# Kernel tuning notes

Hardware: AMD Instinct MI355X
Metric: run time of the kernel (lower is better)

The kernel has to match this reference:

```python
import jax, jax.numpy as jnp
import numpy as np

B, N_O, N_Q = 2, 512, 512
POS_DIM, LATENT, HEADS, HEAD_DIM, OUT_DIM = 3, 256, 8, 32, 128
HD = HEADS * HEAD_DIM  # == LATENT here


def _lin(key, fan_in, fan_out):
    return jax.random.normal(key, (fan_in, fan_out), jnp.float32) / np.sqrt(fan_in)


def setup_inputs() -> dict:
    key = jax.random.key(0)
    ks = jax.random.split(key, 12)
    return {
        'h_obs': jax.random.normal(ks[0], (B, N_O, LATENT), jnp.float32),
        'pos_obs': jax.random.uniform(ks[1], (B, N_O, POS_DIM), jnp.float32),
        'pos_query': jax.random.uniform(ks[2], (B, N_Q, POS_DIM), jnp.float32),
        'fw1': _lin(ks[3], LATENT, LATENT), 'fb1': jnp.zeros((LATENT,), jnp.float32),
        'fw2': _lin(ks[4], LATENT, HD), 'fb2': jnp.zeros((HD,), jnp.float32),
        'log_sigma': jnp.zeros((HEADS,), jnp.float32),
        'kw1': _lin(ks[5], POS_DIM * 3, LATENT), 'kb1': jnp.zeros((LATENT,), jnp.float32),
        'kw2': _lin(ks[6], LATENT, HEADS), 'kb2': jnp.zeros((HEADS,), jnp.float32),
        'ow': _lin(ks[7], HD, OUT_DIM), 'ob': jnp.zeros((OUT_DIM,), jnp.float32),
        'vw': _lin(ks[8], HD, OUT_DIM), 'vb': jnp.zeros((OUT_DIM,), jnp.float32),
    }


def reference(h_obs, pos_obs, pos_query, fw1, fb1, fw2, fb2, log_sigma,
              kw1, kb1, kw2, kb2, ow, ob, vw, vb):
    Bv, No, _ = h_obs.shape
    Nq = pos_query.shape[1]
    # feature net -> values [B, H, N_o, D]
    v = jax.nn.relu(h_obs @ fw1 + fb1) @ fw2 + fb2
    v = v.reshape(Bv, No, HEADS, HEAD_DIM).transpose(0, 2, 1, 3)
    # pairwise relative positions [B, Nq, No, P]
    pos_q = pos_query[:, :, None, :]
    pos_o = pos_obs[:, None, :, :]
    rel = pos_q - pos_o
    dist2 = jnp.sum(rel ** 2, axis=-1)  # [B, Nq, No]
    sigma = jnp.exp(log_sigma)[None, :, None, None]
    rbf = jnp.exp(-dist2[:, None] / (sigma ** 2 + 1e-6))  # [B, H, Nq, No]
    # kernel MLP on concatenated pairwise positions [B, Nq, No, 3P] -> [B, H, Nq, No]
    ki = jnp.concatenate([
        jnp.broadcast_to(pos_q, (Bv, Nq, No, POS_DIM)),
        jnp.broadcast_to(pos_o, (Bv, Nq, No, POS_DIM)),
        rel], axis=-1)
    delta = (jax.nn.relu(ki @ kw1 + kb1) @ kw2 + kb2).transpose(0, 3, 1, 2)
    logits = jnp.log(rbf + 1e-8) + delta
    weights = jax.nn.softmax(logits, axis=-1)  # [B, H, Nq, No]
    # weighted mean over observations
    v_mean = jnp.einsum('bhqo,bhod->bhqd', weights, v)  # [B, H, Nq, D]
    h_query = v_mean.transpose(0, 2, 1, 3).reshape(Bv, Nq, HD)
    # weighted variance: sum_o w * (v_o - v_mean)^2
    residual = v[:, :, None, :, :] - v_mean[:, :, :, None, :]  # [B, H, Nq, No, D]
    var = jnp.sum(weights[..., None] * residual ** 2, axis=3)  # [B, H, Nq, D]
    var = var.transpose(0, 2, 1, 3).reshape(Bv, Nq, HD)
    mean = h_query @ ow + ob
    var_out = jax.nn.softplus(var @ vw + vb)
    return (mean, var_out)
```

## Files before the change

kernel.cpp:

```cpp
#include <hip/hip_runtime.h>
#include <math.h>

#define NB 2
#define NO 512
#define NQ 512
#define OUT_DIM 128
#define LPAD 520

typedef __attribute__((ext_vector_type(8))) short short8;
typedef __attribute__((ext_vector_type(4))) float f32x4;
typedef float v2f __attribute__((ext_vector_type(2)));

__device__ __forceinline__ float softplus_f(float x) {
  return x > 0.0f ? x + log1pf(expf(-x)) : log1pf(expf(x));
}
__device__ __forceinline__ unsigned short bf16_rne(float f) {
  unsigned u = __float_as_uint(f);
  unsigned r = u + 0x7FFFu + ((u >> 16) & 1u);
  return (unsigned short)(r >> 16);
}
__device__ __forceinline__ float bf16_to_f32(unsigned short h) {
  return __uint_as_float(((unsigned)h) << 16);
}
__device__ __forceinline__ unsigned pack_bf2(float x, float y) {
  unsigned ux = __float_as_uint(x);
  unsigned uy = __float_as_uint(y);
  ux = ux + 0x7FFFu + ((ux >> 16) & 1u);
  uy = uy + 0x7FFFu + ((uy >> 16) & 1u);
  return (ux >> 16) | (uy & 0xFFFF0000u);
}
__device__ __forceinline__ v2f unpk_bf2(unsigned u) {
  v2f r; r.x = __uint_as_float(u << 16); r.y = __uint_as_float(u & 0xFFFF0000u);
  return r;
}
__device__ __forceinline__ v2f splat2(float x) { v2f r; r.x = x; r.y = x; return r; }
__device__ __forceinline__ v2f fma2(v2f a, v2f b, v2f c) { return __builtin_elementwise_fma(a, b, c); }
__device__ __forceinline__ v2f max2(v2f a, v2f b) { return __builtin_elementwise_max(a, b); }

__global__ __launch_bounds__(1024) void prep_kernel(
    const float* __restrict__ h_obs, const float* __restrict__ fw1,
    const float* __restrict__ fb1, const float* __restrict__ fw2,
    const float* __restrict__ fb2, const float* __restrict__ pos_obs,
    const float* __restrict__ kw1, unsigned short* __restrict__ V_bf,
    unsigned short* __restrict__ AO_bf)
{
  if (blockIdx.x < 256) {
    __shared__ float s_red[4][4][256];
    __shared__ float s_hid[4][256];
    const int n  = threadIdx.x & 255;
    const int ks = threadIdx.x >> 8;
    const int r0 = blockIdx.x * 4;
    const int k0 = ks * 64;
    float a0 = 0.f, a1 = 0.f, a2 = 0.f, a3 = 0.f;
    #pragma unroll 8
    for (int kk = 0; kk < 64; ++kk) {
      int k = k0 + kk;
      float w = fw1[k * 256 + n];
      a0 = fmaf(h_obs[(r0 + 0) * 256 + k], w, a0);
      a1 = fmaf(h_obs[(r0 + 1) * 256 + k], w, a1);
      a2 = fmaf(h_obs[(r0 + 2) * 256 + k], w, a2);
      a3 = fmaf(h_obs[(r0 + 3) * 256 + k], w, a3);
    }
    s_red[ks][0][n] = a0; s_red[ks][1][n] = a1;
    s_red[ks][2][n] = a2; s_red[ks][3][n] = a3;
    __syncthreads();
    if (ks == 0) {
      float bb = fb1[n];
      #pragma unroll
      for (int r = 0; r < 4; ++r) {
        float v = s_red[0][r][n] + s_red[1][r][n] + s_red[2][r][n] + s_red[3][r][n] + bb;
        s_hid[r][n] = fmaxf(v, 0.f);
      }
    }
    __syncthreads();
    float c0 = 0.f, c1 = 0.f, c2 = 0.f, c3 = 0.f;
    #pragma unroll 8
    for (int kk = 0; kk < 64; ++kk) {
      int k = k0 + kk;
      float w = fw2[k * 256 + n];
      c0 = fmaf(s_hid[0][k], w, c0);
      c1 = fmaf(s_hid[1][k], w, c1);
      c2 = fmaf(s_hid[2][k], w, c2);
      c3 = fmaf(s_hid[3][k], w, c3);
    }
    __syncthreads();
    s_red[ks][0][n] = c0; s_red[ks][1][n] = c1;
    s_red[ks][2][n] = c2; s_red[ks][3][n] = c3;
    __syncthreads();
    if (ks == 0) {
      float bb = fb2[n];
      #pragma unroll
      for (int r = 0; r < 4; ++r) {
        float v = s_red[0][r][n] + s_red[1][r][n] + s_red[2][r][n] + s_red[3][r][n] + bb;
        V_bf[(size_t)(r0 + r) * 256 + n] = bf16_rne(v);
      }
    }
  } else {
    const int i  = blockIdx.x - 256;
    const int b  = i >> 7;
    const int og = i & 127;
    const int ol = threadIdx.x >> 8;
    const int j  = threadIdx.x & 255;
    const int o  = og * 4 + ol;
    float c0 = kw1[3 * 256 + j] - kw1[6 * 256 + j];
    float c1 = kw1[4 * 256 + j] - kw1[7 * 256 + j];
    float c2 = kw1[5 * 256 + j] - kw1[8 * 256 + j];
    const float* p = pos_obs + ((size_t)(b * NO + o)) * 3;
    AO_bf[(size_t)(b * NO + o) * 256 + j] =
        bf16_rne(fmaf(p[0], c0, fmaf(p[1], c1, p[2] * c2)));
  }
}

__global__ __launch_bounds__(512, 4) void attn_fused(
    const unsigned short* __restrict__ V_bf,
    const unsigned short* __restrict__ AO_bf,
    const float* __restrict__ kw1,
    const float* __restrict__ kb1,
    const float* __restrict__ kw2,
    const float* __restrict__ kb2,
    const float* __restrict__ log_sigma,
    const float* __restrict__ pos_obs,
    const float* __restrict__ pos_query,
    const float* __restrict__ ow, const float* __restrict__ obias,
    const float* __restrict__ vw, const float* __restrict__ vbias,
    float* __restrict__ out)
{
  __shared__ float s_logits[2][8 * LPAD];
  __shared__ __align__(16) char poolA[18432];
  __shared__ __align__(16) char poolB[4096];
  __shared__ float s_sum[2][8];

  short8* Bhi    = (short8*)poolA;
  short8* Blo    = (short8*)(poolA + 8192);
  float*  s_redA = (float*)poolA;
  float*  s_pred = (float*)poolA;
  float*  s_aq   = (float*)poolB;
  float*  s_hv   = (float*)poolB;

  const int t   = threadIdx.x;
  const int bq0 = blockIdx.x * 2;
  const int b   = bq0 >> 9;

  float pqx[2], pqy[2], pqz[2];
  #pragma unroll
  for (int q = 0; q < 2; ++q) {
    pqx[q] = pos_query[(bq0 + q) * 3 + 0];
    pqy[q] = pos_query[(bq0 + q) * 3 + 1];
    pqz[q] = pos_query[(bq0 + q) * 3 + 2];
  }
  {
    const int q = t >> 8, j = t & 255;
    float c0 = kw1[0 * 256 + j] + kw1[6 * 256 + j];
    float c1 = kw1[1 * 256 + j] + kw1[7 * 256 + j];
    float c2 = kw1[2 * 256 + j] + kw1[8 * 256 + j];
    s_aq[q * 256 + j] =
        fmaf(pqx[q], c0, fmaf(pqy[q], c1, fmaf(pqz[q], c2, kb1[j])));
  }
  {
    const int o = t;
    const float* p = pos_obs + (size_t)(b * NO + o) * 3;
    float px = p[0], py = p[1], pz = p[2];
    float d2q[2];
    #pragma unroll
    for (int q = 0; q < 2; ++q) {
      float r0 = pqx[q] - px, r1 = pqy[q] - py, r2 = pqz[q] - pz;
      d2q[q] = r0 * r0 + r1 * r1 + r2 * r2;
    }
    #pragma unroll
    for (int h = 0; h < 8; ++h) {
      float sg  = expf(log_sigma[h]);
      float inv = 1.0f / (sg * sg + 1e-6f);
      float kbv = kb2[h];
      s_logits[0][h * LPAD + o] = logf(expf(-d2q[0] * inv) + 1e-8f) + kbv;
      s_logits[1][h * LPAD + o] = logf(expf(-d2q[1] * inv) + 1e-8f) + kbv;
    }
  }
  {
    const int kstep = t >> 6, lane = t & 63;
    const int nh = lane & 15;
    const int kb_ = kstep * 32 + ((lane >> 4) & 3) * 8;
    short8 hi8, lo8;
    #pragma unroll
    for (int i = 0; i < 8; ++i) {
      float v = (nh < 8) ? kw2[(kb_ + i) * 8 + nh] : 0.f;
      unsigned short h = bf16_rne(v);
      hi8[i] = (short)h;
      lo8[i] = (short)bf16_rne(v - bf16_to_f32(h));
    }
    Bhi[kstep * 64 + lane] = hi8;
    Blo[kstep * 64 + lane] = lo8;
  }
  __syncthreads();

  {
    const int wave = t >> 6, lane = t & 63;
    const int quad = lane >> 4, mrow = lane & 15;
    const int tb   = wave * 4;
    f32x4 C[2][4];
    #pragma unroll
    for (int q = 0; q < 2; ++q)
      #pragma unroll
      for (int jt = 0; jt < 4; ++jt) C[q][jt] = (f32x4){0.f, 0.f, 0.f, 0.f};

    for (int kstep = 0; kstep < 8; ++kstep) {
      const int koff = kstep * 32 + quad * 8;
      const v2f* aqp0 = (const v2f*)(s_aq + koff);
      const v2f* aqp1 = (const v2f*)(s_aq + 256 + koff);
      v2f aq0[4], aq1[4];
      #pragma unroll
      for (int i = 0; i < 4; ++i) { aq0[i] = aqp0[i]; aq1[i] = aqp1[i]; }
      short8 bhi = Bhi[kstep * 64 + lane];
      short8 blo = Blo[kstep * 64 + lane];
      #pragma unroll
      for (int jt = 0; jt < 4; ++jt) {
        const int o = (tb + jt) * 16 + mrow;
        int4 u = *(const int4*)(AO_bf + ((size_t)(b * NO + o) << 8) + koff);
        v2f ao[4];
        ao[0] = unpk_bf2((unsigned)u.x); ao[1] = unpk_bf2((unsigned)u.y);
        ao[2] = unpk_bf2((unsigned)u.z); ao[3] = unpk_bf2((unsigned)u.w);
        v2f z = splat2(0.f);
        int4 af0, af1;
        {
          v2f h0 = max2(aq0[0] + ao[0], z), h1 = max2(aq0[1] + ao[1], z);
          v2f h2 = max2(aq0[2] + ao[2], z), h3 = max2(aq0[3] + ao[3], z);
          af0.x = (int)pack_bf2(h0.x, h0.y); af0.y = (int)pack_bf2(h1.x, h1.y);
          af0.z = (int)pack_bf2(h2.x, h2.y); af0.w = (int)pack_bf2(h3.x, h3.y);
        }
        {
          v2f h0 = max2(aq1[0] + ao[0], z), h1 = max2(aq1[1] + ao[1], z);
          v2f h2 = max2(aq1[2] + ao[2], z), h3 = max2(aq1[3] + ao[3], z);
          af1.x = (int)pack_bf2(h0.x, h0.y); af1.y = (int)pack_bf2(h1.x, h1.y);
          af1.z = (int)pack_bf2(h2.x, h2.y); af1.w = (int)pack_bf2(h3.x, h3.y);
        }
        short8 a0 = __builtin_bit_cast(short8, af0);
        short8 a1 = __builtin_bit_cast(short8, af1);
        C[0][jt] = __builtin_amdgcn_mfma_f32_16x16x32_bf16(a0, bhi, C[0][jt], 0, 0, 0);
        C[0][jt] = __builtin_amdgcn_mfma_f32_16x16x32_bf16(a0, blo, C[0][jt], 0, 0, 0);
        C[1][jt] = __builtin_amdgcn_mfma_f32_16x16x32_bf16(a1, bhi, C[1][jt], 0, 0, 0);
        C[1][jt] = __builtin_amdgcn_mfma_f32_16x16x32_bf16(a1, blo, C[1][jt], 0, 0, 0);
      }
    }
    const int h = lane & 15;
    if (h < 8) {
      #pragma unroll
      for (int q = 0; q < 2; ++q)
        #pragma unroll
        for (int jt = 0; jt < 4; ++jt) {
          const int ob = (tb + jt) * 16 + quad * 4;
          #pragma unroll
          for (int r = 0; r < 4; ++r)
            s_logits[q][h * LPAD + ob + r] += C[q][jt][r];
        }
    }
  }
  __syncthreads();

  {
    const int wave = t >> 6, lane = t & 63;
    #pragma unroll
    for (int cc = 0; cc < 2; ++cc) {
      const int c = wave * 2 + cc;
      const int q = c >> 3, h = c & 7;
      float* pl = &s_logits[q][h * LPAD];
      float l[8];
      float m = -1e30f;
      #pragma unroll
      for (int k = 0; k < 8; ++k) {
        l[k] = pl[k * 64 + lane];
        m = fmaxf(m, l[k]);
      }
      #pragma unroll
      for (int off = 32; off >= 1; off >>= 1) m = fmaxf(m, __shfl_xor(m, off, 64));
      float s = 0.f;
      #pragma unroll
      for (int k = 0; k < 8; ++k) {
        float p = expf(l[k] - m);
        pl[k * 64 + lane] = p;
        s += p;
      }
      #pragma unroll
      for (int off = 32; off >= 1; off >>= 1) s += __shfl_xor(s, off, 64);
      if (lane == 0) s_sum[q][h] = s;
    }
  }
  __syncthreads();

  float q1p[8];
  {
    const int s  = t >> 6;
    const int r  = t & 63;
    const int h  = r >> 3, dg = r & 7;
    const unsigned short* vb_ = V_bf + ((size_t)(b * NO) << 8) + h * 32 + dg * 4;
    const float* P0 = &s_logits[0][h * LPAD];
    const float* P1 = &s_logits[1][h * LPAD];
    v2f s1a0 = splat2(0.f), s1b0 = splat2(0.f), s2a0 = splat2(0.f), s2b0 = splat2(0.f);
    v2f s1a1 = splat2(0.f), s1b1 = splat2(0.f), s2a1 = splat2(0.f), s2b1 = splat2(0.f);
    const int o0 = s * 64;
    #pragma unroll 4
    for (int oi = 0; oi < 64; ++oi) {
      const int o = o0 + oi;
      uint2 vv = *(const uint2*)(vb_ + ((size_t)o << 8));
      v2f va  = unpk_bf2(vv.x);
      v2f vb2 = unpk_bf2(vv.y);
      v2f p0 = splat2(P0[o]), p1 = splat2(P1[o]);
      s1a0 = fma2(p0, va, s1a0);  s1b0 = fma2(p0, vb2, s1b0);
      v2f t0a = p0 * va, t0b = p0 * vb2;
      s2a0 = fma2(t0a, va, s2a0); s2b0 = fma2(t0b, vb2, s2b0);
      s1a1 = fma2(p1, va, s1a1);  s1b1 = fma2(p1, vb2, s1b1);
      v2f t1a = p1 * va, t1b = p1 * vb2;
      s2a1 = fma2(t1a, va, s2a1); s2b1 = fma2(t1b, vb2, s2b1);
    }
    float* row = s_redA + t * 9;
    row[0] = s1a0.x; row[1] = s1a0.y; row[2] = s1b0.x; row[3] = s1b0.y;
    row[4] = s2a0.x; row[5] = s2a0.y; row[6] = s2b0.x; row[7] = s2b0.y;
    q1p[0] = s1a1.x; q1p[1] = s1a1.y; q1p[2] = s1b1.x; q1p[3] = s1b1.y;
    q1p[4] = s2a1.x; q1p[5] = s2a1.y; q1p[6] = s2b1.x; q1p[7] = s2b1.y;
  }
  __syncthreads();
  if (t < 256) {
    const int hd = t, h = hd >> 5, d = hd & 31, dg = d >> 2, c = d & 3;
    float S1 = 0.f, S2 = 0.f;
    #pragma unroll
    for (int s = 0; s < 8; ++s) {
      const float* row = s_redA + (size_t)(s * 64 + h * 8 + dg) * 9;
      S1 += row[c]; S2 += row[4 + c];
    }
    float inv = 1.0f / s_sum[0][h];
    float m1 = S1 * inv;
    float va = fmaxf(S2 * inv - m1 * m1, 0.f);
    s_hv[0 * 256 + hd] = m1;
    s_hv[1 * 256 + hd] = va;
  }
  __syncthreads();
  {
    float* row = s_redA + t * 9;
    #pragma unroll
    for (int i = 0; i < 8; ++i) row[i] = q1p[i];
  }
  __syncthreads();
  if (t < 256) {
    const int hd = t, h = hd >> 5, d = hd & 31, dg = d >> 2, c = d & 3;
    float S1 = 0.f, S2 = 0.f;
    #pragma unroll
    for (int s = 0; s < 8; ++s) {
      const float* row = s_redA + (size_t)(s * 64 + h * 8 + dg) * 9;
      S1 += row[c]; S2 += row[4 + c];
    }
    float inv = 1.0f / s_sum[1][h];
    float m1 = S1 * inv;
    float va = fmaxf(S2 * inv - m1 * m1, 0.f);
    s_hv[2 * 256 + hd] = m1;
    s_hv[3 * 256 + hd] = va;
  }
  __syncthreads();

  {
    const int ks = t >> 8, mode = (t >> 7) & 1, n = t & 127;
    const float* W  = mode ? vw : ow;
    const float* X0 = s_hv + mode * 256;
    const float* X1 = s_hv + (2 + mode) * 256;
    float a0 = 0.f, a1 = 0.f;
    const int k0 = ks * 128;
    #pragma unroll 4
    for (int k = k0; k < k0 + 128; k += 4) {
      float4 x0 = *(const float4*)&X0[k];
      float4 x1 = *(const float4*)&X1[k];
      float w0 = W[(k + 0) * 128 + n];
      float w1 = W[(k + 1) * 128 + n];
      float w2 = W[(k + 2) * 128 + n];
      float w3 = W[(k + 3) * 128 + n];
      a0 = fmaf(x0.x, w0, a0); a1 = fmaf(x1.x, w0, a1);
      a0 = fmaf(x0.y, w1, a0); a1 = fmaf(x1.y, w1, a1);
      a0 = fmaf(x0.z, w2, a0); a1 = fmaf(x1.z, w2, a1);
      a0 = fmaf(x0.w, w3, a0); a1 = fmaf(x1.w, w3, a1);
    }
    __syncthreads();
    s_pred[((ks * 2 + mode) * 2 + 0) * 128 + n] = a0;
    s_pred[((ks * 2 + mode) * 2 + 1) * 128 + n] = a1;
  }
  __syncthreads();
  {
    const int q = t >> 8, mode = (t >> 7) & 1, n = t & 127;
    float v = s_pred[((0 * 2 + mode) * 2 + q) * 128 + n]
            + s_pred[((1 * 2 + mode) * 2 + q) * 128 + n]
            + (mode ? vbias[n] : obias[n]);
    if (mode) v = softplus_f(v);
    out[(size_t)mode * (NB * NQ * OUT_DIM) + (size_t)(bq0 + q) * OUT_DIM + n] = v;
  }
}

extern "C" void kernel_launch(void* const* d_in, const int* in_sizes, int n_in,
                              void* d_out, int out_size, void* d_ws, size_t ws_size,
                              hipStream_t stream)
{
  const float* h_obs     = (const float*)d_in[0];
  const float* pos_obs   = (const float*)d_in[1];
  const float* pos_query = (const float*)d_in[2];
  const float* fw1       = (const float*)d_in[3];
  const float* fb1       = (const float*)d_in[4];
  const float* fw2       = (const float*)d_in[5];
  const float* fb2       = (const float*)d_in[6];
  const float* log_sigma = (const float*)d_in[7];
  const float* kw1       = (const float*)d_in[8];
  const float* kb1       = (const float*)d_in[9];
  const float* kw2       = (const float*)d_in[10];
  const float* kb2       = (const float*)d_in[11];
  const float* ow        = (const float*)d_in[12];
  const float* ob        = (const float*)d_in[13];
  const float* vw        = (const float*)d_in[14];
  const float* vb        = (const float*)d_in[15];

  float* out = (float*)d_out;
  unsigned short* ws = (unsigned short*)d_ws;

  unsigned short* V_bf  = ws;
  unsigned short* AO_bf = ws + 262144;

  prep_kernel<<<512, 1024, 0, stream>>>(h_obs, fw1, fb1, fw2, fb2,
                                        pos_obs, kw1, V_bf, AO_bf);
  attn_fused<<<NB * NQ / 2, 512, 0, stream>>>(V_bf, AO_bf, kw1, kb1, kw2, kb2,
                                              log_sigma, pos_obs, pos_query,
                                              ow, ob, vw, vb, out);
}
```

Measured before the change: 148.6 us.

## Shrink shared memory and retune prep and attention kernels for occupancy

The prep kernel is reorganized into 1024 blocks of 512 threads, each handling two rows instead of four. The attention kernel raises its launch-bounds occupancy hint to 6 and trims shared memory by changing LPAD and poolA size. It also caches the per-head sigma and bias terms in shared memory, vectorizes the probability loads as float4, and switches the partial-sum reduction to a column-major layout. Other changes include a hardware packed-bf16 conversion builtin and moving one barrier. These target occupancy and LDS bank conflicts, but the occupancy hint risks register spills.

```diff
diff --git a/kernel.cpp b/kernel.cpp
--- a/kernel.cpp
+++ b/kernel.cpp
@@ -5,7 +5,7 @@
 #define NO 512
 #define NQ 512
 #define OUT_DIM 128
-#define LPAD 520
+#define LPAD 516
 
 typedef __attribute__((ext_vector_type(8))) short short8;
 typedef __attribute__((ext_vector_type(4))) float f32x4;
@@ -22,12 +22,25 @@
 __device__ __forceinline__ float bf16_to_f32(unsigned short h) {
   return __uint_as_float(((unsigned)h) << 16);
 }
+
+#if defined(__has_builtin)
+#if __has_builtin(__builtin_amdgcn_cvt_pk_bf16_f32)
+#define HAS_CVT_PK_BF16 1
+#endif
+#endif
+
 __device__ __forceinline__ unsigned pack_bf2(float x, float y) {
+#ifdef HAS_CVT_PK_BF16
+  auto r = __builtin_amdgcn_cvt_pk_bf16_f32(x, y);
+  unsigned u; __builtin_memcpy(&u, &r, 4);
+  return u;
+#else
   unsigned ux = __float_as_uint(x);
   unsigned uy = __float_as_uint(y);
   ux = ux + 0x7FFFu + ((ux >> 16) & 1u);
   uy = uy + 0x7FFFu + ((uy >> 16) & 1u);
   return (ux >> 16) | (uy & 0xFFFF0000u);
+#endif
 }
 __device__ __forceinline__ v2f unpk_bf2(unsigned u) {
   v2f r; r.x = __uint_as_float(u << 16); r.y = __uint_as_float(u & 0xFFFF0000u);
@@ -37,71 +50,59 @@
 __device__ __forceinline__ v2f fma2(v2f a, v2f b, v2f c) { return __builtin_elementwise_fma(a, b, c); }
 __device__ __forceinline__ v2f max2(v2f a, v2f b) { return __builtin_elementwise_max(a, b); }
 
-__global__ __launch_bounds__(1024) void prep_kernel(
+__global__ __launch_bounds__(512) void prep_kernel(
     const float* __restrict__ h_obs, const float* __restrict__ fw1,
     const float* __restrict__ fb1, const float* __restrict__ fw2,
     const float* __restrict__ fb2, const float* __restrict__ pos_obs,
     const float* __restrict__ kw1, unsigned short* __restrict__ V_bf,
     unsigned short* __restrict__ AO_bf)
 {
-  if (blockIdx.x < 256) {
-    __shared__ float s_red[4][4][256];
-    __shared__ float s_hid[4][256];
+  if (blockIdx.x < 512) {
+    __shared__ float s_red[2][2][256];
+    __shared__ float s_hid[2][256];
     const int n  = threadIdx.x & 255;
     const int ks = threadIdx.x >> 8;
-    const int r0 = blockIdx.x * 4;
-    const int k0 = ks * 64;
-    float a0 = 0.f, a1 = 0.f, a2 = 0.f, a3 = 0.f;
+    const int r0 = blockIdx.x * 2;
+    const int k0 = ks * 128;
+    float a0 = 0.f, a1 = 0.f;
     #pragma unroll 8
-    for (int kk = 0; kk < 64; ++kk) {
+    for (int kk = 0; kk < 128; ++kk) {
       int k = k0 + kk;
       float w = fw1[k * 256 + n];
       a0 = fmaf(h_obs[(r0 + 0) * 256 + k], w, a0);
       a1 = fmaf(h_obs[(r0 + 1) * 256 + k], w, a1);
-      a2 = fmaf(h_obs[(r0 + 2) * 256 + k], w, a2);
-      a3 = fmaf(h_obs[(r0 + 3) * 256 + k], w, a3);
     }
     s_red[ks][0][n] = a0; s_red[ks][1][n] = a1;
-    s_red[ks][2][n] = a2; s_red[ks][3][n] = a3;
     __syncthreads();
     if (ks == 0) {
       float bb = fb1[n];
-      #pragma unroll
-      for (int r = 0; r < 4; ++r) {
-        float v = s_red[0][r][n] + s_red[1][r][n] + s_red[2][r][n] + s_red[3][r][n] + bb;
-        s_hid[r][n] = fmaxf(v, 0.f);
-      }
+      s_hid[0][n] = fmaxf(s_red[0][0][n] + s_red[1][0][n] + bb, 0.f);
+      s_hid[1][n] = fmaxf(s_red[0][1][n] + s_red[1][1][n] + bb, 0.f);
     }
     __syncthreads();
-    float c0 = 0.f, c1 = 0.f, c2 = 0.f, c3 = 0.f;
+    float c0 = 0.f, c1 = 0.f;
     #pragma unroll 8
-    for (int kk = 0; kk < 64; ++kk) {
+    for (int kk = 0; kk < 128; ++kk) {
       int k = k0 + kk;
       float w = fw2[k * 256 + n];
       c0 = fmaf(s_hid[0][k], w, c0);
       c1 = fmaf(s_hid[1][k], w, c1);
-      c2 = fmaf(s_hid[2][k], w, c2);
-      c3 = fmaf(s_hid[3][k], w, c3);
     }
     __syncthreads();
     s_red[ks][0][n] = c0; s_red[ks][1][n] = c1;
-    s_red[ks][2][n] = c2; s_red[ks][3][n] = c3;
     __syncthreads();
     if (ks == 0) {
       float bb = fb2[n];
-      #pragma unroll
-      for (int r = 0; r < 4; ++r) {
-        float v = s_red[0][r][n] + s_red[1][r][n] + s_red[2][r][n] + s_red[3][r][n] + bb;
-        V_bf[(size_t)(r0 + r) * 256 + n] = bf16_rne(v);
-      }
+      V_bf[(size_t)(r0 + 0) * 256 + n] = bf16_rne(s_red[0][0][n] + s_red[1][0][n] + bb);
+      V_bf[(size_t)(r0 + 1) * 256 + n] = bf16_rne(s_red[0][1][n] + s_red[1][1][n] + bb);
     }
   } else {
-    const int i  = blockIdx.x - 256;
-    const int b  = i >> 7;
-    const int og = i & 127;
-    const int ol = threadIdx.x >> 8;
-    const int j  = threadIdx.x & 255;
-    const int o  = og * 4 + ol;
+    const int i     = blockIdx.x - 512;
+    const int b     = i >> 8;
+    const int chunk = i & 255;
+    const int ol    = threadIdx.x >> 8;
+    const int j     = threadIdx.x & 255;
+    const int o     = chunk * 2 + ol;
     float c0 = kw1[3 * 256 + j] - kw1[6 * 256 + j];
     float c1 = kw1[4 * 256 + j] - kw1[7 * 256 + j];
     float c2 = kw1[5 * 256 + j] - kw1[8 * 256 + j];
@@ -111,7 +112,7 @@
   }
 }
 
-__global__ __launch_bounds__(512, 4) void attn_fused(
+__global__ __launch_bounds__(512, 6) void attn_fused(
     const unsigned short* __restrict__ V_bf,
     const unsigned short* __restrict__ AO_bf,
     const float* __restrict__ kw1,
@@ -126,13 +127,15 @@
     float* __restrict__ out)
 {
   __shared__ float s_logits[2][8 * LPAD];
-  __shared__ __align__(16) char poolA[18432];
+  __shared__ __align__(16) char poolA[16512];
   __shared__ __align__(16) char poolB[4096];
   __shared__ float s_sum[2][8];
+  __shared__ float s_invs2[8];
+  __shared__ float s_kb2v[8];
 
   short8* Bhi    = (short8*)poolA;
   short8* Blo    = (short8*)(poolA + 8192);
-  float*  s_redA = (float*)poolA;
+  float*  s_redC = (float*)poolA;
   float*  s_pred = (float*)poolA;
   float*  s_aq   = (float*)poolB;
   float*  s_hv   = (float*)poolB;
@@ -157,25 +160,6 @@
         fmaf(pqx[q], c0, fmaf(pqy[q], c1, fmaf(pqz[q], c2, kb1[j])));
   }
   {
-    const int o = t;
-    const float* p = pos_obs + (size_t)(b * NO + o) * 3;
-    float px = p[0], py = p[1], pz = p[2];
-    float d2q[2];
-    #pragma unroll
-    for (int q = 0; q < 2; ++q) {
-      float r0 = pqx[q] - px, r1 = pqy[q] - py, r2 = pqz[q] - pz;
-      d2q[q] = r0 * r0 + r1 * r1 + r2 * r2;
-    }
-    #pragma unroll
-    for (int h = 0; h < 8; ++h) {
-      float sg  = expf(log_sigma[h]);
-      float inv = 1.0f / (sg * sg + 1e-6f);
-      float kbv = kb2[h];
-      s_logits[0][h * LPAD + o] = logf(expf(-d2q[0] * inv) + 1e-8f) + kbv;
-      s_logits[1][h * LPAD + o] = logf(expf(-d2q[1] * inv) + 1e-8f) + kbv;
-    }
-  }
-  {
     const int kstep = t >> 6, lane = t & 63;
     const int nh = lane & 15;
     const int kb_ = kstep * 32 + ((lane >> 4) & 3) * 8;
@@ -190,7 +174,31 @@
     Bhi[kstep * 64 + lane] = hi8;
     Blo[kstep * 64 + lane] = lo8;
   }
-  __syncthreads();
+  if (t < 8) {
+    float s = expf(log_sigma[t]);
+    s_invs2[t] = 1.0f / (s * s + 1e-6f);
+    s_kb2v[t]  = kb2[t];
+  }
+  __syncthreads();
+
+  {
+    const int o = t;
+    const float* p = pos_obs + (size_t)(b * NO + o) * 3;
+    float px = p[0], py = p[1], pz = p[2];
+    float d2q[2];
+    #pragma unroll
+    for (int q = 0; q < 2; ++q) {
+      float r0 = pqx[q] - px, r1 = pqy[q] - py, r2 = pqz[q] - pz;
+      d2q[q] = r0 * r0 + r1 * r1 + r2 * r2;
+    }
+    #pragma unroll
+    for (int h = 0; h < 8; ++h) {
+      float inv = s_invs2[h];
+      float kbv = s_kb2v[h];
+      s_logits[0][h * LPAD + o] = logf(expf(-d2q[0] * inv) + 1e-8f) + kbv;
+      s_logits[1][h * LPAD + o] = logf(expf(-d2q[1] * inv) + 1e-8f) + kbv;
+    }
+  }
 
   {
     const int wave = t >> 6, lane = t & 63;
@@ -240,6 +248,8 @@
         C[1][jt] = __builtin_amdgcn_mfma_f32_16x16x32_bf16(a1, blo, C[1][jt], 0, 0, 0);
       }
     }
+    __syncthreads();
+
     const int h = lane & 15;
     if (h < 8) {
       #pragma unroll
@@ -291,28 +301,34 @@
     const int r  = t & 63;
     const int h  = r >> 3, dg = r & 7;
     const unsigned short* vb_ = V_bf + ((size_t)(b * NO) << 8) + h * 32 + dg * 4;
-    const float* P0 = &s_logits[0][h * LPAD];
-    const float* P1 = &s_logits[1][h * LPAD];
+    const float* P0 = &s_logits[0][h * LPAD + s * 64];
+    const float* P1 = &s_logits[1][h * LPAD + s * 64];
     v2f s1a0 = splat2(0.f), s1b0 = splat2(0.f), s2a0 = splat2(0.f), s2b0 = splat2(0.f);
     v2f s1a1 = splat2(0.f), s1b1 = splat2(0.f), s2a1 = splat2(0.f), s2b1 = splat2(0.f);
     const int o0 = s * 64;
-    #pragma unroll 4
-    for (int oi = 0; oi < 64; ++oi) {
-      const int o = o0 + oi;
-      uint2 vv = *(const uint2*)(vb_ + ((size_t)o << 8));
-      v2f va  = unpk_bf2(vv.x);
-      v2f vb2 = unpk_bf2(vv.y);
-      v2f p0 = splat2(P0[o]), p1 = splat2(P1[o]);
-      s1a0 = fma2(p0, va, s1a0);  s1b0 = fma2(p0, vb2, s1b0);
-      v2f t0a = p0 * va, t0b = p0 * vb2;
-      s2a0 = fma2(t0a, va, s2a0); s2b0 = fma2(t0b, vb2, s2b0);
-      s1a1 = fma2(p1, va, s1a1);  s1b1 = fma2(p1, vb2, s1b1);
-      v2f t1a = p1 * va, t1b = p1 * vb2;
-      s2a1 = fma2(t1a, va, s2a1); s2b1 = fma2(t1b, vb2, s2b1);
-    }
-    float* row = s_redA + t * 9;
-    row[0] = s1a0.x; row[1] = s1a0.y; row[2] = s1b0.x; row[3] = s1b0.y;
-    row[4] = s2a0.x; row[5] = s2a0.y; row[6] = s2b0.x; row[7] = s2b0.y;
+    #pragma unroll 2
+    for (int oi = 0; oi < 64; oi += 4) {
+      float4 pv0 = *(const float4*)&P0[oi];
+      float4 pv1 = *(const float4*)&P1[oi];
+      #pragma unroll
+      for (int i = 0; i < 4; ++i) {
+        const int o = o0 + oi + i;
+        uint2 vv = *(const uint2*)(vb_ + ((size_t)o << 8));
+        v2f va  = unpk_bf2(vv.x);
+        v2f vb2 = unpk_bf2(vv.y);
+        v2f p0 = splat2((&pv0.x)[i]), p1 = splat2((&pv1.x)[i]);
+        s1a0 = fma2(p0, va, s1a0);  s1b0 = fma2(p0, vb2, s1b0);
+        v2f t0a = p0 * va, t0b = p0 * vb2;
+        s2a0 = fma2(t0a, va, s2a0); s2b0 = fma2(t0b, vb2, s2b0);
+        s1a1 = fma2(p1, va, s1a1);  s1b1 = fma2(p1, vb2, s1b1);
+        v2f t1a = p1 * va, t1b = p1 * vb2;
+        s2a1 = fma2(t1a, va, s2a1); s2b1 = fma2(t1b, vb2, s2b1);
+      }
+    }
+    s_redC[0 * LPAD + t] = s1a0.x; s_redC[1 * LPAD + t] = s1a0.y;
+    s_redC[2 * LPAD + t] = s1b0.x; s_redC[3 * LPAD + t] = s1b0.y;
+    s_redC[4 * LPAD + t] = s2a0.x; s_redC[5 * LPAD + t] = s2a0.y;
+    s_redC[6 * LPAD + t] = s2b0.x; s_redC[7 * LPAD + t] = s2b0.y;
     q1p[0] = s1a1.x; q1p[1] = s1a1.y; q1p[2] = s1b1.x; q1p[3] = s1b1.y;
     q1p[4] = s2a1.x; q1p[5] = s2a1.y; q1p[6] = s2b1.x; q1p[7] = s2b1.y;
   }
@@ -322,8 +338,9 @@
     float S1 = 0.f, S2 = 0.f;
     #pragma unroll
     for (int s = 0; s < 8; ++s) {
-      const float* row = s_redA + (size_t)(s * 64 + h * 8 + dg) * 9;
-      S1 += row[c]; S2 += row[4 + c];
+      const int idx = s * 64 + h * 8 + dg;
+      S1 += s_redC[c * LPAD + idx];
+      S2 += s_redC[(4 + c) * LPAD + idx];
     }
     float inv = 1.0f / s_sum[0][h];
     float m1 = S1 * inv;
@@ -333,9 +350,8 @@
   }
   __syncthreads();
   {
-    float* row = s_redA + t * 9;
-    #pragma unroll
-    for (int i = 0; i < 8; ++i) row[i] = q1p[i];
+    #pragma unroll
+    for (int i = 0; i < 8; ++i) s_redC[i * LPAD + t] = q1p[i];
   }
   __syncthreads();
   if (t < 256) {
@@ -343,8 +359,9 @@
     float S1 = 0.f, S2 = 0.f;
     #pragma unroll
     for (int s = 0; s < 8; ++s) {
-      const float* row = s_redA + (size_t)(s * 64 + h * 8 + dg) * 9;
-      S1 += row[c]; S2 += row[4 + c];
+      const int idx = s * 64 + h * 8 + dg;
+      S1 += s_redC[c * LPAD + idx];
+      S2 += s_redC[(4 + c) * LPAD + idx];
     }
     float inv = 1.0f / s_sum[1][h];
     float m1 = S1 * inv;
@@ -374,7 +391,6 @@
       a0 = fmaf(x0.z, w2, a0); a1 = fmaf(x1.z, w2, a1);
       a0 = fmaf(x0.w, w3, a0); a1 = fmaf(x1.w, w3, a1);
     }
-    __syncthreads();
     s_pred[((ks * 2 + mode) * 2 + 0) * 128 + n] = a0;
     s_pred[((ks * 2 + mode) * 2 + 1) * 128 + n] = a1;
   }
@@ -416,7 +432,7 @@
   unsigned short* V_bf  = ws;
   unsigned short* AO_bf = ws + 262144;
 
-  prep_kernel<<<512, 1024, 0, stream>>>(h_obs, fw1, fb1, fw2, fb2,
+  prep_kernel<<<1024, 512, 0, stream>>>(h_obs, fw1, fb1, fw2, fb2,
                                         pos_obs, kw1, V_bf, AO_bf);
   attn_fused<<<NB * NQ / 2, 512, 0, stream>>>(V_bf, AO_bf, kw1, kb1, kw2, kb2,
                                               log_sigma, pos_obs, pos_query,
```

Measured after the change: 154.2 us. 3.8% more time.
